# Performance work log

Measured on AMD Instinct MI355X. Metric: run time of the kernel, lower is better.

Reference implementation:

```python
import jax, jax.numpy as jnp
import numpy as np

NUM_HEADS = 16
EPS = 1e-5


def _layernorm(x, w):
    # torch LayerNorm (biased variance), bias=False
    m = jnp.mean(x, axis=-1, keepdims=True)
    v = jnp.mean(jnp.square(x - m), axis=-1, keepdims=True)
    return (x - m) * jax.lax.rsqrt(v + EPS) * w


def setup_inputs() -> dict:
    key = jax.random.key(0)
    ks = jax.random.split(key, 8)
    B, S, H, A = 2, 2048, 1024, 1024
    hd = H // NUM_HEADS
    return {
        "x": jax.random.normal(ks[0], (B, S, H), jnp.float32),
        "ada_cond": jax.random.normal(ks[1], (B, A), jnp.float32),
        "freqs": jax.random.normal(ks[2], (S, hd // 2, 2), jnp.float32),
        "w_qkv": jax.random.normal(ks[3], (3 * H, H), jnp.float32) * (1.0 / np.sqrt(H)),
        "w_o": jax.random.normal(ks[4], (H, H), jnp.float32) * (1.0 / np.sqrt(H)),
        "ln_w": jnp.ones((H,), jnp.float32),
        "mod_w": jax.random.normal(ks[5], (3 * H, A), jnp.float32) * 0.02,
        "mod_b": jax.random.normal(ks[6], (3 * H,), jnp.float32) * 0.02,
        "qn_w": jnp.ones((hd,), jnp.float32),
        "kn_w": jnp.ones((hd,), jnp.float32),
    }


def reference(x, ada_cond, freqs, w_qkv, w_o, ln_w, mod_w, mod_b, qn_w, kn_w):
    B, S, H = x.shape
    nh = NUM_HEADS
    hd = H // nh

    # pre-norm + AdaLN modulation (with gate)
    h = _layernorm(x, ln_w)
    mod = (jax.nn.silu(ada_cond) @ mod_w.T + mod_b)[:, None, :]  # [B,1,3H]
    scale, shift, gate = jnp.split(mod, 3, axis=-1)
    h = h * (scale + 1.0) + shift

    # QKV projection and head split
    qkv = h @ w_qkv.T                                  # [B,S,3H]
    q, k, v = jnp.split(qkv, 3, axis=-1)
    to_heads = lambda t: t.reshape(B, S, nh, hd).transpose(0, 2, 1, 3)  # [B,nh,S,hd]
    q, k, v = to_heads(q), to_heads(k), to_heads(v)

    # per-head QK layernorm
    q = _layernorm(q, qn_w)
    k = _layernorm(k, kn_w)

    # RoPE (complex rotation via interleaved pairs)
    f = freqs[:S].reshape(1, 1, S, hd // 2, 2)

    def rope(t):
        tr = t.reshape(B, nh, S, hd // 2, 2)
        re = tr[..., 0] * f[..., 0] - tr[..., 1] * f[..., 1]
        im = tr[..., 1] * f[..., 0] + tr[..., 0] * f[..., 1]
        return jnp.stack([re, im], axis=-1).reshape(B, nh, S, hd)

    q, k = rope(q), rope(k)

    # scaled dot-product attention (non-causal)
    scores = jnp.einsum("bhqd,bhkd->bhqk", q, k) * (1.0 / np.sqrt(hd))
    attn = jax.nn.softmax(scores, axis=-1)
    o = jnp.einsum("bhqk,bhkd->bhqd", attn, v)
    o = o.transpose(0, 2, 1, 3).reshape(B, S, H)

    return (o @ w_o.T) * gate
```

## Files before the change

### kernel.cpp

```cpp
#include <hip/hip_runtime.h>
#include <hip/hip_bf16.h>
#include <hip/hip_fp16.h>
#include <math.h>

#define B_ 2
#define S_ 2048
#define H_ 1024
#define A_ 1024
#define NH_ 16
#define HD_ 64
#define H3_ 3072
#define EPS_ 1e-5f

typedef __attribute__((ext_vector_type(8))) short short8;
typedef __attribute__((ext_vector_type(4))) float floatx4;
typedef __attribute__((ext_vector_type(4))) _Float16 half4v;
typedef __attribute__((ext_vector_type(2))) __fp16 fp16x2;

__device__ inline unsigned short f2bf(float x) {
    union { float f; unsigned u; } v; v.f = x;
    unsigned r = v.u + 0x7fffu + ((v.u >> 16) & 1u);
    return (unsigned short)(r >> 16);
}

__device__ inline unsigned pk_bf16(float a, float b) {
    union { __hip_bfloat162 h; unsigned u; } v;
    v.h = __float22bfloat162_rn(make_float2(a, b));
    return v.u;
}

__device__ inline unsigned pk_f16(float a, float b) {
    union { __half2 h; unsigned u; } v;
    v.h = __float22half2_rn(make_float2(a, b));
    return v.u;
}

__device__ inline void gld_lds16(const void* g, void* l) {
    __builtin_amdgcn_global_load_lds(
        (const __attribute__((address_space(1))) unsigned int*)g,
        (__attribute__((address_space(3))) unsigned int*)l, 16, 0, 0);
}

__global__ __launch_bounds__(256) void cast_bf16_kernel(
    const float* __restrict__ in, unsigned short* __restrict__ out, int n)
{
    int i = (blockIdx.x * 256 + threadIdx.x) * 8;
    if (i >= n) return;
    float4 a = *(const float4*)(in + i);
    float4 b = *(const float4*)(in + i + 4);
    uint4 o;
    o.x = pk_bf16(a.x, a.y);
    o.y = pk_bf16(a.z, a.w);
    o.z = pk_bf16(b.x, b.y);
    o.w = pk_bf16(b.z, b.w);
    *(uint4*)(out + i) = o;
}

__global__ __launch_bounds__(256) void mod_gemv_kernel(
    const float* __restrict__ ada, const float* __restrict__ mod_w,
    const float* __restrict__ mod_b, float* __restrict__ mod)
{
    int wid = threadIdx.x >> 6;
    int lane = threadIdx.x & 63;
    int idx = blockIdx.x * 4 + wid;
    int b = idx / H3_;
    int j = idx % H3_;
    const float* ar = ada + (size_t)b * A_;
    const float* wr = mod_w + (size_t)j * A_;
    float acc = 0.f;
    for (int a = lane; a < A_; a += 64) {
        float av = ar[a];
        float sv = av / (1.f + __expf(-av));
        acc += sv * wr[a];
    }
    #pragma unroll
    for (int m = 1; m < 64; m <<= 1) acc += __shfl_xor(acc, m);
    if (lane == 0) mod[idx] = acc + mod_b[j];
}

__global__ __launch_bounds__(256) void ln_mod_kernel(
    const float* __restrict__ x, const float* __restrict__ ln_w,
    const float* __restrict__ mod, unsigned short* __restrict__ hout)
{
    int row = blockIdx.x;
    int b = row >> 11;
    const float* xr = x + (size_t)row * H_;
    int t = threadIdx.x;
    float4 xv = *(const float4*)(xr + t * 4);
    float s1 = xv.x + xv.y + xv.z + xv.w;
    float s2 = xv.x*xv.x + xv.y*xv.y + xv.z*xv.z + xv.w*xv.w;
    #pragma unroll
    for (int m = 1; m < 64; m <<= 1) { s1 += __shfl_xor(s1, m); s2 += __shfl_xor(s2, m); }
    __shared__ float r1[4], r2[4];
    int wid = t >> 6, lane = t & 63;
    if (lane == 0) { r1[wid] = s1; r2[wid] = s2; }
    __syncthreads();
    s1 = r1[0] + r1[1] + r1[2] + r1[3];
    s2 = r2[0] + r2[1] + r2[2] + r2[3];
    float mean = s1 * (1.f / H_);
    float var  = s2 * (1.f / H_) - mean * mean;
    float rstd = rsqrtf(var + EPS_);
    const float* mrow = mod + (size_t)b * H3_;
    float4 wv = *(const float4*)(ln_w + t * 4);
    float4 sc = *(const float4*)(mrow + t * 4);
    float4 sh = *(const float4*)(mrow + H_ + t * 4);
    float4 hv;
    hv.x = (xv.x - mean) * rstd * wv.x * (sc.x + 1.f) + sh.x;
    hv.y = (xv.y - mean) * rstd * wv.y * (sc.y + 1.f) + sh.y;
    hv.z = (xv.z - mean) * rstd * wv.z * (sc.z + 1.f) + sh.z;
    hv.w = (xv.w - mean) * rstd * wv.w * (sc.w + 1.f) + sh.w;
    uint2 o;
    o.x = pk_bf16(hv.x, hv.y);
    o.y = pk_bf16(hv.z, hv.w);
    *(uint2*)(hout + (size_t)row * H_ + t * 4) = o;
}

__global__ __launch_bounds__(256) void gemm_qkv_fused_kernel(
    const unsigned short* __restrict__ A, const unsigned short* __restrict__ Bm,
    const float* __restrict__ freqs, const float* __restrict__ qn_w,
    const float* __restrict__ kn_w, unsigned short* __restrict__ qout,
    unsigned short* __restrict__ kout, unsigned short* __restrict__ vtout)
{
    __shared__ unsigned short As[2][128 * 32];
    __shared__ unsigned short Bs[2][128 * 32];
    const int K = H_;
    int t = threadIdx.x;
    int w = t >> 6, lane = t & 63;
    int q16 = lane & 15, quad = lane >> 4;
    int wm = w >> 1, wn = w & 1;
    int m0 = blockIdx.y * 128, n0 = blockIdx.x * 128;

    int srow = 2 * (lane >> 3) + ((lane >> 2) & 1);
    int scol = ((lane & 3) ^ ((lane >> 3) & 3)) << 3;
    const unsigned short* ga = A + (size_t)(m0 + (w << 5) + srow) * K + scol;
    const unsigned short* gb = Bm + (size_t)(n0 + (w << 5) + srow) * K + scol;
    int ldst0 = (w * 16) * 64;
    int ldst1 = (w * 16 + 8) * 64;

    floatx4 acc[4][4];
    #pragma unroll
    for (int mt = 0; mt < 4; ++mt)
        #pragma unroll
        for (int nt = 0; nt < 4; ++nt)
            acc[mt][nt] = (floatx4){0.f, 0.f, 0.f, 0.f};

    int abase = (wm * 32 + (q16 >> 1)) * 64 + (q16 & 1) * 32
              + ((quad ^ ((q16 >> 1) & 3)) << 3);
    int bbase = (wn * 32 + (q16 >> 1)) * 64 + (q16 & 1) * 32
              + ((quad ^ ((q16 >> 1) & 3)) << 3);

    gld_lds16(ga, &As[0][ldst0]);
    gld_lds16(ga + (size_t)16 * K, &As[0][ldst1]);
    gld_lds16(gb, &Bs[0][ldst0]);
    gld_lds16(gb + (size_t)16 * K, &Bs[0][ldst1]);
    __syncthreads();

    int cur = 0;
    for (int kt = 0; kt < K / 32; ++kt) {
        const unsigned short* curA = &As[cur][0];
        const unsigned short* curB = &Bs[cur][0];
        short8 af[4], bf[4];
        #pragma unroll
        for (int mt = 0; mt < 4; ++mt)
            af[mt] = *(const short8*)&curA[abase + mt * 512];
        #pragma unroll
        for (int nt = 0; nt < 4; ++nt)
            bf[nt] = *(const short8*)&curB[bbase + nt * 512];

        if (kt + 1 < K / 32) {
            const unsigned short* ga2 = ga + (kt + 1) * 32;
            const unsigned short* gb2 = gb + (kt + 1) * 32;
            int nb = cur ^ 1;
            gld_lds16(ga2, &As[nb][ldst0]);
            gld_lds16(ga2 + (size_t)16 * K, &As[nb][ldst1]);
            gld_lds16(gb2, &Bs[nb][ldst0]);
            gld_lds16(gb2 + (size_t)16 * K, &Bs[nb][ldst1]);
        }

        #pragma unroll
        for (int mt = 0; mt < 4; ++mt)
            #pragma unroll
            for (int nt = 0; nt < 4; ++nt)
                acc[mt][nt] = __builtin_amdgcn_mfma_f32_16x16x32_bf16(
                    af[mt], bf[nt], acc[mt][nt], 0, 0, 0);

        __syncthreads();
        cur ^= 1;
    }

    int n_base = n0 + wn * 64;
    int sec = n_base >> 10;
    int head = (n_base & 1023) >> 6;

    if (sec == 2) {
        #pragma unroll
        for (int mt = 0; mt < 4; ++mt) {
            int m = m0 + wm * 64 + mt * 16 + quad * 4;
            int b = m >> 11, s = m & (S_ - 1);
            #pragma unroll
            for (int nt = 0; nt < 4; ++nt) {
                int d = nt * 16 + q16;
                unsigned short* dst =
                    vtout + ((size_t)((b * 16 + head) * 64 + d)) * S_ + s;
                uint2 pk;
                pk.x = pk_f16(acc[mt][nt][0], acc[mt][nt][1]);
                pk.y = pk_f16(acc[mt][nt][2], acc[mt][nt][3]);
                *(uint2*)dst = pk;
            }
        }
    } else {
        const float* nw = (sec == 0) ? qn_w : kn_w;
        float w4[4];
        #pragma unroll
        for (int nt = 0; nt < 4; ++nt) w4[nt] = nw[nt * 16 + q16];
        unsigned short* outp = (sec == 0) ? qout : kout;
        float qscale = (sec == 0) ? 0.1803368801111244f : 1.0f;

        #pragma unroll
        for (int mt = 0; mt < 4; ++mt) {
            #pragma unroll
            for (int i = 0; i < 4; ++i) {
                int m = m0 + wm * 64 + mt * 16 + quad * 4 + i;
                int b = m >> 11, s = m & (S_ - 1);
                float v0 = acc[mt][0][i], v1 = acc[mt][1][i];
                float v2 = acc[mt][2][i], v3 = acc[mt][3][i];
                float s1 = (v0 + v1) + (v2 + v3);
                float s2 = (v0 * v0 + v1 * v1) + (v2 * v2 + v3 * v3);
                #pragma unroll
                for (int msk = 1; msk < 16; msk <<= 1) {
                    s1 += __shfl_xor(s1, msk);
                    s2 += __shfl_xor(s2, msk);
                }
                float mean = s1 * (1.f / 64);
                float var  = s2 * (1.f / 64) - mean * mean;
                float rstd = rsqrtf(var + EPS_);
                float vv[4];
                vv[0] = (v0 - mean) * rstd * w4[0];
                vv[1] = (v1 - mean) * rstd * w4[1];
                vv[2] = (v2 - mean) * rstd * w4[2];
                vv[3] = (v3 - mean) * rstd * w4[3];
                const float* fr = freqs + (size_t)s * 64;
                unsigned short* orow = outp + ((size_t)((b * 16 + head) * S_ + s)) * 64;
                #pragma unroll
                for (int nt = 0; nt < 4; ++nt) {
                    int c = nt * 16 + q16;
                    float vp = __shfl_xor(vv[nt], 1);
                    float2 ff = *(const float2*)(fr + (c & ~1));
                    float r = (c & 1) ? (vv[nt] * ff.x + vp * ff.y)
                                      : (vv[nt] * ff.x - vp * ff.y);
                    orow[c] = f2bf(r * qscale);
                }
            }
        }
    }
}

__global__ __launch_bounds__(256) void gemm_bt_bf16_kernel(
    const unsigned short* __restrict__ A, const unsigned short* __restrict__ Bm,
    float* __restrict__ C, int M, int N, int K,
    const float* __restrict__ gate, int gate_stride, int batch_shift)
{
    __shared__ unsigned short As[2][128 * 32];
    __shared__ unsigned short Bs[2][64 * 32];
    int t = threadIdx.x;
    int w = t >> 6, lane = t & 63;
    int q16 = lane & 15, quad = lane >> 4;
    int m0 = blockIdx.y * 128, n0 = blockIdx.x * 64;

    int srow = 2 * (lane >> 3) + ((lane >> 2) & 1);
    int scol = ((lane & 3) ^ ((lane >> 3) & 3)) << 3;
    const unsigned short* ga = A + (size_t)(m0 + (w << 5) + srow) * K + scol;
    const unsigned short* gb = Bm + (size_t)(n0 + (w << 4) + srow) * K + scol;
    int ldstA0 = (w * 16) * 64;
    int ldstA1 = (w * 16 + 8) * 64;
    int ldstB  = (w * 8) * 64;

    floatx4 acc[2][4];
    #pragma unroll
    for (int mt = 0; mt < 2; ++mt)
        #pragma unroll
        for (int nt = 0; nt < 4; ++nt)
            acc[mt][nt] = (floatx4){0.f, 0.f, 0.f, 0.f};

    int abase = (w * 16 + (q16 >> 1)) * 64 + (q16 & 1) * 32
              + ((quad ^ ((q16 >> 1) & 3)) << 3);
    int bbase = (q16 >> 1) * 64 + (q16 & 1) * 32
              + ((quad ^ ((q16 >> 1) & 3)) << 3);

    gld_lds16(ga, &As[0][ldstA0]);
    gld_lds16(ga + (size_t)16 * K, &As[0][ldstA1]);
    gld_lds16(gb, &Bs[0][ldstB]);
    __syncthreads();

    int cur = 0;
    for (int kt = 0; kt < K / 32; ++kt) {
        const unsigned short* curA = &As[cur][0];
        const unsigned short* curB = &Bs[cur][0];
        short8 af[2], bf[4];
        #pragma unroll
        for (int mt = 0; mt < 2; ++mt)
            af[mt] = *(const short8*)&curA[abase + mt * 512];
        #pragma unroll
        for (int nt = 0; nt < 4; ++nt)
            bf[nt] = *(const short8*)&curB[bbase + nt * 512];

        if (kt + 1 < K / 32) {
            const unsigned short* ga2 = ga + (kt + 1) * 32;
            const unsigned short* gb2 = gb + (kt + 1) * 32;
            int nb = cur ^ 1;
            gld_lds16(ga2, &As[nb][ldstA0]);
            gld_lds16(ga2 + (size_t)16 * K, &As[nb][ldstA1]);
            gld_lds16(gb2, &Bs[nb][ldstB]);
        }

        #pragma unroll
        for (int mt = 0; mt < 2; ++mt)
            #pragma unroll
            for (int nt = 0; nt < 4; ++nt)
                acc[mt][nt] = __builtin_amdgcn_mfma_f32_16x16x32_bf16(
                    af[mt], bf[nt], acc[mt][nt], 0, 0, 0);

        __syncthreads();
        cur ^= 1;
    }

    #pragma unroll
    for (int mt = 0; mt < 2; ++mt) {
        #pragma unroll
        for (int i = 0; i < 4; ++i) {
            int m = m0 + w * 32 + mt * 16 + quad * 4 + i;
            float* crow = C + (size_t)m * N;
            const float* grow = gate ? gate + (size_t)(m >> batch_shift) * gate_stride
                                     : nullptr;
            #pragma unroll
            for (int nt = 0; nt < 4; ++nt) {
                int n = n0 + nt * 16 + q16;
                float v = acc[mt][nt][i];
                if (gate) v *= grow[n];
                crow[n] = v;
            }
        }
    }
}

__global__ __launch_bounds__(256, 2) void attn_mfma_kernel(
    const unsigned short* __restrict__ q, const unsigned short* __restrict__ k,
    const unsigned short* __restrict__ vt, unsigned short* __restrict__ o)
{
    __shared__ __align__(16) unsigned char smem[16 * 1024];
    __shared__ float lbuf[4][4][16];
    unsigned short* Vs = (unsigned short*)smem;

    int t = threadIdx.x;
    int w = t >> 6, lane = t & 63;
    int q16 = lane & 15, quad = lane >> 4;
    int bh = blockIdx.y, b = bh >> 4, h = bh & 15;
    int s0 = blockIdx.x * 64;

    const unsigned short* qgp = q + ((size_t)bh * S_ + s0) * HD_;
    short8 qf[4][2];
    #pragma unroll
    for (int qg = 0; qg < 4; ++qg)
        #pragma unroll
        for (int hh = 0; hh < 2; ++hh)
            qf[qg][hh] = *(const short8*)(qgp + (16 * qg + q16) * HD_ + hh * 32 + quad * 8);

    const unsigned short* kg = k + (size_t)bh * S_ * HD_ + (16 * w + q16) * HD_ + quad * 8;

    const unsigned short* vg0 = vt + (size_t)bh * 64 * S_
                              + (size_t)(16 * w + (lane >> 3)) * S_ + (lane & 7) * 8;
    const unsigned short* vg1 = vg0 + 8 * S_;
    unsigned short* vw0 = Vs + (16 * w + (lane >> 3)) * 64 + (((lane & 7) ^ (lane >> 3)) << 3);
    unsigned short* vw1 = vw0 + 512;
    int vroff = q16 * 64 + (((2 * w + (quad >> 1)) ^ (q16 & 7)) << 3) + ((quad & 1) << 2);

    const int NT = S_ / 64;

    short8 kf_nx0 = *(const short8*)kg;
    short8 kf_nx1 = *(const short8*)(kg + 32);
    uint4 vr0 = *(const uint4*)vg0;
    uint4 vr1 = *(const uint4*)vg1;
    vg0 += 64; vg1 += 64;

    *(uint4*)vw0 = vr0;
    *(uint4*)vw1 = vr1;
    vr0 = *(const uint4*)vg0;
    vr1 = *(const uint4*)vg1;
    vg0 += 64; vg1 += 64;
    __syncthreads();

    union { half4v h; uint2 u; } ones;
    ones.u.x = 0x3C003C00u; ones.u.y = 0x3C003C00u;

    floatx4 acc_o[4][4];
    floatx4 acc_l[4];
    #pragma unroll
    for (int nd = 0; nd < 4; ++nd)
        #pragma unroll
        for (int qg = 0; qg < 4; ++qg)
            acc_o[nd][qg] = (floatx4){0.f, 0.f, 0.f, 0.f};
    #pragma unroll
    for (int qg = 0; qg < 4; ++qg) acc_l[qg] = (floatx4){0.f, 0.f, 0.f, 0.f};

    int cur = 0;
    for (int kt = 0; kt < NT; ++kt) {
        short8 kf0 = kf_nx0, kf1 = kf_nx1;

        if (kt + 1 < NT) {
            int nb = cur ^ 1;
            *(uint4*)(vw0 + nb * 4096) = vr0;
            *(uint4*)(vw1 + nb * 4096) = vr1;
            kg += 64 * HD_;
            kf_nx0 = *(const short8*)kg;
            kf_nx1 = *(const short8*)(kg + 32);
            if (kt + 2 < NT) {
                vr0 = *(const uint4*)vg0;
                vr1 = *(const uint4*)vg1;
                vg0 += 64; vg1 += 64;
            }
        }

        floatx4 sc[4];
        #pragma unroll
        for (int qg = 0; qg < 4; ++qg) sc[qg] = (floatx4){-12.f, -12.f, -12.f, -12.f};
        #pragma unroll
        for (int qg = 0; qg < 4; ++qg) {
            sc[qg] = __builtin_amdgcn_mfma_f32_16x16x32_bf16(kf0, qf[qg][0], sc[qg], 0, 0, 0);
            sc[qg] = __builtin_amdgcn_mfma_f32_16x16x32_bf16(kf1, qf[qg][1], sc[qg], 0, 0, 0);
        }

        const unsigned short* vbase = Vs + cur * 4096;
        half4v vf[4];
        #pragma unroll
        for (int nd = 0; nd < 4; ++nd)
            vf[nd] = *(const half4v*)&vbase[vroff + nd * 1024];

        #pragma unroll
        for (int qg = 0; qg < 4; ++qg) {
            float p0 = __builtin_amdgcn_exp2f(sc[qg][0]);
            float p1 = __builtin_amdgcn_exp2f(sc[qg][1]);
            float p2 = __builtin_amdgcn_exp2f(sc[qg][2]);
            float p3 = __builtin_amdgcn_exp2f(sc[qg][3]);
            union { half4v h; fp16x2 f2[2]; } pf;
            pf.f2[0] = __builtin_amdgcn_cvt_pkrtz(p0, p1);
            pf.f2[1] = __builtin_amdgcn_cvt_pkrtz(p2, p3);
            acc_l[qg] = __builtin_amdgcn_mfma_f32_16x16x16f16(ones.h, pf.h, acc_l[qg], 0, 0, 0);
            #pragma unroll
            for (int nd = 0; nd < 4; ++nd)
                acc_o[nd][qg] = __builtin_amdgcn_mfma_f32_16x16x16f16(
                    vf[nd], pf.h, acc_o[nd][qg], 0, 0, 0);
        }

        __syncthreads();
        cur ^= 1;
    }

    if (quad == 0) {
        #pragma unroll
        for (int qg = 0; qg < 4; ++qg) lbuf[w][qg][q16] = acc_l[qg][0];
    }
    __syncthreads();
    float linv = 1.f / (lbuf[0][w][q16] + lbuf[1][w][q16] + lbuf[2][w][q16] + lbuf[3][w][q16]);

    float* obuf = (float*)smem;
    float* myw = obuf + ((w * 4) * 64 + lane) * 4;
    float* myr = obuf + (w * 64 + lane) * 4;
    unsigned short* og = o + ((size_t)(b * S_ + s0 + 16 * w + q16)) * H_ + h * HD_ + 4 * quad;

    #pragma unroll
    for (int nd = 0; nd < 4; ++nd) {
        __syncthreads();
        #pragma unroll
        for (int qg = 0; qg < 4; ++qg)
            *(floatx4*)(myw + qg * 256) = acc_o[nd][qg];
        __syncthreads();
        floatx4 r0 = *(const floatx4*)(myr);
        floatx4 r1 = *(const floatx4*)(myr + 1024);
        floatx4 r2 = *(const floatx4*)(myr + 2048);
        floatx4 r3 = *(const floatx4*)(myr + 3072);
        floatx4 s = (r0 + r1) + (r2 + r3);
        uint2 pk;
        pk.x = pk_bf16(s[0] * linv, s[1] * linv);
        pk.y = pk_bf16(s[2] * linv, s[3] * linv);
        *(uint2*)(og + nd * 16) = pk;
    }
}

extern "C" void kernel_launch(void* const* d_in, const int* in_sizes, int n_in,
                              void* d_out, int out_size, void* d_ws, size_t ws_size,
                              hipStream_t stream)
{
    const float* x     = (const float*)d_in[0];
    const float* ada   = (const float*)d_in[1];
    const float* freqs = (const float*)d_in[2];
    const float* w_qkv = (const float*)d_in[3];
    const float* w_o   = (const float*)d_in[4];
    const float* ln_w  = (const float*)d_in[5];
    const float* mod_w = (const float*)d_in[6];
    const float* mod_b = (const float*)d_in[7];
    const float* qn_w  = (const float*)d_in[8];
    const float* kn_w  = (const float*)d_in[9];
    float* out = (float*)d_out;

    float* ws  = (float*)d_ws;
    float* mod = ws;
    unsigned short* hb    = (unsigned short*)(mod + 8192);
    unsigned short* qb    = hb + (size_t)B_ * S_ * H_;
    unsigned short* kb    = qb + (size_t)B_ * S_ * H_;
    unsigned short* vtb   = kb + (size_t)B_ * S_ * H_;
    unsigned short* ob    = vtb + (size_t)B_ * S_ * H_;
    unsigned short* wqkvb = ob + (size_t)B_ * S_ * H_;
    unsigned short* wob   = wqkvb + (size_t)H3_ * H_;

    cast_bf16_kernel<<<H3_ * H_ / (8 * 256), 256, 0, stream>>>(w_qkv, wqkvb, H3_ * H_);
    cast_bf16_kernel<<<H_ * H_ / (8 * 256), 256, 0, stream>>>(w_o, wob, H_ * H_);
    mod_gemv_kernel<<<B_ * H3_ / 4, 256, 0, stream>>>(ada, mod_w, mod_b, mod);
    ln_mod_kernel<<<B_ * S_, 256, 0, stream>>>(x, ln_w, mod, hb);
    gemm_qkv_fused_kernel<<<dim3(H3_ / 128, B_ * S_ / 128), 256, 0, stream>>>(
        hb, wqkvb, freqs, qn_w, kn_w, qb, kb, vtb);
    attn_mfma_kernel<<<dim3(S_ / 64, B_ * NH_), 256, 0, stream>>>(qb, kb, vtb, ob);
    gemm_bt_bf16_kernel<<<dim3(H_ / 64, B_ * S_ / 128), 256, 0, stream>>>(
        ob, wob, out, B_ * S_, H_, H_, mod + 2 * H_, H3_, 11);
}
```

Before: 253.6 us.

## Use triple-buffered LDS pipelines with explicit vmcnt waits in GEMMs

Both GEMM kernels move from a double-buffered LDS scheme to a three-stage ring. Loads are issued two tiles ahead, and partial s_waitcnt vmcnt counts let in-flight global->LDS copies overlap the MFMA work instead of draining at every __syncthreads. The attention kernel swaps __syncthreads for an lgkmcnt wait plus a raw s_barrier wrapped in sched_barriers, which avoids an unnecessary vmcnt drain so the V prefetch can stay in flight. The cost is extra LDS per block, which may reduce occupancy, and the hand-counted waitcnts become fragile if the compiler emits other memory ops.

```diff
diff --git a/kernel.cpp b/kernel.cpp
--- a/kernel.cpp
+++ b/kernel.cpp
@@ -40,6 +40,9 @@
         (const __attribute__((address_space(1))) unsigned int*)g,
         (__attribute__((address_space(3))) unsigned int*)l, 16, 0, 0);
 }
+
+#define SFENCE() __builtin_amdgcn_sched_barrier(0)
+#define RAW_BARRIER() do { SFENCE(); __builtin_amdgcn_s_barrier(); SFENCE(); } while (0)
 
 __global__ __launch_bounds__(256) void cast_bf16_kernel(
     const float* __restrict__ in, unsigned short* __restrict__ out, int n)
@@ -121,9 +124,10 @@
     const float* __restrict__ kn_w, unsigned short* __restrict__ qout,
     unsigned short* __restrict__ kout, unsigned short* __restrict__ vtout)
 {
-    __shared__ unsigned short As[2][128 * 32];
-    __shared__ unsigned short Bs[2][128 * 32];
+    __shared__ unsigned short As[3][128 * 32];
+    __shared__ unsigned short Bs[3][128 * 32];
     const int K = H_;
+    const int NIT = K / 32;
     int t = threadIdx.x;
     int w = t >> 6, lane = t & 63;
     int q16 = lane & 15, quad = lane >> 4;
@@ -149,16 +153,23 @@
     int bbase = (wn * 32 + (q16 >> 1)) * 64 + (q16 & 1) * 32
               + ((quad ^ ((q16 >> 1) & 3)) << 3);
 
-    gld_lds16(ga, &As[0][ldst0]);
-    gld_lds16(ga + (size_t)16 * K, &As[0][ldst1]);
-    gld_lds16(gb, &Bs[0][ldst0]);
-    gld_lds16(gb + (size_t)16 * K, &Bs[0][ldst1]);
-    __syncthreads();
-
-    int cur = 0;
-    for (int kt = 0; kt < K / 32; ++kt) {
-        const unsigned short* curA = &As[cur][0];
-        const unsigned short* curB = &Bs[cur][0];
+    #pragma unroll
+    for (int p = 0; p < 3; ++p) {
+        gld_lds16(ga + p * 32, &As[p][ldst0]);
+        gld_lds16(ga + p * 32 + (size_t)16 * K, &As[p][ldst1]);
+        gld_lds16(gb + p * 32, &Bs[p][ldst0]);
+        gld_lds16(gb + p * 32 + (size_t)16 * K, &Bs[p][ldst1]);
+    }
+
+    int cb = 0;
+    for (int kt = 0; kt < NIT; ++kt) {
+        if (kt < NIT - 2)       asm volatile("s_waitcnt vmcnt(8)" ::: "memory");
+        else if (kt == NIT - 2) asm volatile("s_waitcnt vmcnt(4)" ::: "memory");
+        else                    asm volatile("s_waitcnt vmcnt(0)" ::: "memory");
+        RAW_BARRIER();
+
+        const unsigned short* curA = &As[cb][0];
+        const unsigned short* curB = &Bs[cb][0];
         short8 af[4], bf[4];
         #pragma unroll
         for (int mt = 0; mt < 4; ++mt)
@@ -166,16 +177,6 @@
         #pragma unroll
         for (int nt = 0; nt < 4; ++nt)
             bf[nt] = *(const short8*)&curB[bbase + nt * 512];
-
-        if (kt + 1 < K / 32) {
-            const unsigned short* ga2 = ga + (kt + 1) * 32;
-            const unsigned short* gb2 = gb + (kt + 1) * 32;
-            int nb = cur ^ 1;
-            gld_lds16(ga2, &As[nb][ldst0]);
-            gld_lds16(ga2 + (size_t)16 * K, &As[nb][ldst1]);
-            gld_lds16(gb2, &Bs[nb][ldst0]);
-            gld_lds16(gb2 + (size_t)16 * K, &Bs[nb][ldst1]);
-        }
 
         #pragma unroll
         for (int mt = 0; mt < 4; ++mt)
@@ -184,8 +185,18 @@
                 acc[mt][nt] = __builtin_amdgcn_mfma_f32_16x16x32_bf16(
                     af[mt], bf[nt], acc[mt][nt], 0, 0, 0);
 
-        __syncthreads();
-        cur ^= 1;
+        asm volatile("s_waitcnt lgkmcnt(0)" ::: "memory");
+        RAW_BARRIER();
+
+        if (kt + 3 < NIT) {
+            const unsigned short* ga2 = ga + (kt + 3) * 32;
+            const unsigned short* gb2 = gb + (kt + 3) * 32;
+            gld_lds16(ga2, &As[cb][ldst0]);
+            gld_lds16(ga2 + (size_t)16 * K, &As[cb][ldst1]);
+            gld_lds16(gb2, &Bs[cb][ldst0]);
+            gld_lds16(gb2 + (size_t)16 * K, &Bs[cb][ldst1]);
+        }
+        cb = (cb == 2) ? 0 : cb + 1;
     }
 
     int n_base = n0 + wn * 64;
@@ -260,8 +271,9 @@
     float* __restrict__ C, int M, int N, int K,
     const float* __restrict__ gate, int gate_stride, int batch_shift)
 {
-    __shared__ unsigned short As[2][128 * 32];
-    __shared__ unsigned short Bs[2][64 * 32];
+    __shared__ unsigned short As[3][128 * 32];
+    __shared__ unsigned short Bs[3][64 * 32];
+    const int NIT = 1024 / 32;
     int t = threadIdx.x;
     int w = t >> 6, lane = t & 63;
     int q16 = lane & 15, quad = lane >> 4;
@@ -287,15 +299,22 @@
     int bbase = (q16 >> 1) * 64 + (q16 & 1) * 32
               + ((quad ^ ((q16 >> 1) & 3)) << 3);
 
-    gld_lds16(ga, &As[0][ldstA0]);
-    gld_lds16(ga + (size_t)16 * K, &As[0][ldstA1]);
-    gld_lds16(gb, &Bs[0][ldstB]);
-    __syncthreads();
-
-    int cur = 0;
-    for (int kt = 0; kt < K / 32; ++kt) {
-        const unsigned short* curA = &As[cur][0];
-        const unsigned short* curB = &Bs[cur][0];
+    #pragma unroll
+    for (int p = 0; p < 3; ++p) {
+        gld_lds16(ga + p * 32, &As[p][ldstA0]);
+        gld_lds16(ga + p * 32 + (size_t)16 * K, &As[p][ldstA1]);
+        gld_lds16(gb + p * 32, &Bs[p][ldstB]);
+    }
+
+    int cb = 0;
+    for (int kt = 0; kt < NIT; ++kt) {
+        if (kt < NIT - 2)       asm volatile("s_waitcnt vmcnt(6)" ::: "memory");
+        else if (kt == NIT - 2) asm volatile("s_waitcnt vmcnt(3)" ::: "memory");
+        else                    asm volatile("s_waitcnt vmcnt(0)" ::: "memory");
+        RAW_BARRIER();
+
+        const unsigned short* curA = &As[cb][0];
+        const unsigned short* curB = &Bs[cb][0];
         short8 af[2], bf[4];
         #pragma unroll
         for (int mt = 0; mt < 2; ++mt)
@@ -303,15 +322,6 @@
         #pragma unroll
         for (int nt = 0; nt < 4; ++nt)
             bf[nt] = *(const short8*)&curB[bbase + nt * 512];
-
-        if (kt + 1 < K / 32) {
-            const unsigned short* ga2 = ga + (kt + 1) * 32;
-            const unsigned short* gb2 = gb + (kt + 1) * 32;
-            int nb = cur ^ 1;
-            gld_lds16(ga2, &As[nb][ldstA0]);
-            gld_lds16(ga2 + (size_t)16 * K, &As[nb][ldstA1]);
-            gld_lds16(gb2, &Bs[nb][ldstB]);
-        }
 
         #pragma unroll
         for (int mt = 0; mt < 2; ++mt)
@@ -320,8 +330,17 @@
                 acc[mt][nt] = __builtin_amdgcn_mfma_f32_16x16x32_bf16(
                     af[mt], bf[nt], acc[mt][nt], 0, 0, 0);
 
-        __syncthreads();
-        cur ^= 1;
+        asm volatile("s_waitcnt lgkmcnt(0)" ::: "memory");
+        RAW_BARRIER();
+
+        if (kt + 3 < NIT) {
+            const unsigned short* ga2 = ga + (kt + 3) * 32;
+            const unsigned short* gb2 = gb + (kt + 3) * 32;
+            gld_lds16(ga2, &As[cb][ldstA0]);
+            gld_lds16(ga2 + (size_t)16 * K, &As[cb][ldstA1]);
+            gld_lds16(gb2, &Bs[cb][ldstB]);
+        }
+        cb = (cb == 2) ? 0 : cb + 1;
     }
 
     #pragma unroll
@@ -387,7 +406,8 @@
     vr0 = *(const uint4*)vg0;
     vr1 = *(const uint4*)vg1;
     vg0 += 64; vg1 += 64;
-    __syncthreads();
+    asm volatile("s_waitcnt lgkmcnt(0)" ::: "memory");
+    RAW_BARRIER();
 
     union { half4v h; uint2 u; } ones;
     ones.u.x = 0x3C003C00u; ones.u.y = 0x3C003C00u;
@@ -451,7 +471,8 @@
                     vf[nd], pf.h, acc_o[nd][qg], 0, 0, 0);
         }
 
-        __syncthreads();
+        asm volatile("s_waitcnt lgkmcnt(0)" ::: "memory");
+        RAW_BARRIER();
         cur ^= 1;
     }
 
```

Result: faster. 247.9 us (-2.3%).
